# Kernel tuning notes

Hardware: AMD Instinct MI355X
Metric: run time of the kernel (lower is better)

Reference implementation:

```python
import jax, jax.numpy as jnp
import numpy as np

B, S, D_IN, D_EMB, H = 2, 2048, 1024, 1024, 16
HD = D_EMB // H

def setup_inputs() -> dict:
    key = jax.random.key(0)
    k1, k2, k3 = jax.random.split(key, 3)
    # xavier-uniform style scales
    lim_qkv = float(np.sqrt(6.0 / (D_IN + 3 * D_EMB)))
    lim_o = float(np.sqrt(6.0 / (D_EMB + D_EMB)))
    return {
        "x": jax.random.normal(k1, (B, S, D_IN), dtype=jnp.float32),
        "W_qkv": jax.random.uniform(k2, (3 * D_EMB, D_IN), minval=-lim_qkv, maxval=lim_qkv, dtype=jnp.float32),
        "b_qkv": jnp.zeros((3 * D_EMB,), dtype=jnp.float32),
        "W_o": jax.random.uniform(k3, (D_EMB, D_EMB), minval=-lim_o, maxval=lim_o, dtype=jnp.float32),
        "b_o": jnp.zeros((D_EMB,), dtype=jnp.float32),
    }

def reference(x, W_qkv, b_qkv, W_o, b_o):
    b, s, _ = x.shape
    qkv = x @ W_qkv.T + b_qkv                     # [B,S,3E]
    qkv = qkv.reshape(b, s, H, 3 * HD).transpose(0, 2, 1, 3)  # [B,H,S,3*HD]
    q, k, v = jnp.split(qkv, 3, axis=-1)          # each [B,H,S,HD]
    scale = 1.0 / np.sqrt(HD)
    attn = jax.nn.softmax(jnp.einsum('bhqd,bhkd->bhqk', q, k) * scale, axis=-1)
    vals = jnp.einsum('bhqk,bhkd->bhqd', attn, v) # [B,H,S,HD]
    vals = vals.transpose(0, 2, 1, 3).reshape(b, s, D_EMB)
    return vals @ W_o.T + b_o
```

## Files before the change

### kernel.cpp

```cpp
#include <hip/hip_runtime.h>
#include <hip/hip_bf16.h>

typedef unsigned short u16;
typedef unsigned int u32;
typedef __bf16 bf16x8 __attribute__((ext_vector_type(8)));
typedef float f32x4 __attribute__((ext_vector_type(4)));
typedef u32 u32x4 __attribute__((ext_vector_type(4)));

#define MFMA16(a, b, c) __builtin_amdgcn_mfma_f32_16x16x32_bf16((a), (b), (c), 0, 0, 0)

static __device__ __forceinline__ u16 f2bf(float f) {
  __hip_bfloat16 h = __float2bfloat16(f);
  return __builtin_bit_cast(u16, h);
}

static __device__ __forceinline__ u32 pack2(float a, float b) {
  return (u32)f2bf(a) | ((u32)f2bf(b) << 16);
}

static __device__ __forceinline__ bf16x8 ldbf8(const void* p) {
  return *reinterpret_cast<const bf16x8*>(p);
}

static __device__ __forceinline__ void gload_lds16(const void* g, void* l) {
  __builtin_amdgcn_global_load_lds(
      (const __attribute__((address_space(1))) u32*)g,
      (__attribute__((address_space(3))) u32*)l, 16, 0, 0);
}

__global__ void cvt_all(const float* __restrict__ x, const float* __restrict__ wq,
                        const float* __restrict__ wo, u16* __restrict__ xb,
                        u16* __restrict__ wqb, u16* __restrict__ wob) {
  int i = blockIdx.x * 256 + threadIdx.x;
  const float* s;
  u16* d;
  int j;
  if (i < 524288) {
    s = x; d = xb; j = i;
  } else if (i < 917504) {
    s = wq; d = wqb; j = i - 524288;
  } else {
    s = wo; d = wob; j = i - 917504;
  }
  const float4* p = reinterpret_cast<const float4*>(s) + (size_t)j * 2;
  float4 a = p[0], b = p[1];
  uint4 o;
  o.x = (u32)f2bf(a.x) | ((u32)f2bf(a.y) << 16);
  o.y = (u32)f2bf(a.z) | ((u32)f2bf(a.w) << 16);
  o.z = (u32)f2bf(b.x) | ((u32)f2bf(b.y) << 16);
  o.w = (u32)f2bf(b.z) | ((u32)f2bf(b.w) << 16);
  reinterpret_cast<uint4*>(d)[j] = o;
}

template <bool BF16OUT>
__global__ __launch_bounds__(256, 3) void gemm_bt(const u16* __restrict__ A,
                                                  const u16* __restrict__ Bm,
                                                  const float* __restrict__ bias,
                                                  void* __restrict__ Cp,
                                                  int M, int N, int K) {
  __shared__ __align__(16) char As[128 * 64 * 2];
  __shared__ __align__(16) char Bs[128 * 64 * 2];
  const int tid = threadIdx.x;
  const int lane = tid & 63;
  const int wid = tid >> 6;
  const int fr = lane & 15, fg = lane >> 4;
  const int gx = gridDim.x, nwg = gx * gridDim.y;
  const int id = blockIdx.y * gx + blockIdx.x;
  const int nid = (id & 7) * (nwg >> 3) + (id >> 3);
  const int bm = nid / gx, bn = nid % gx;
  const int wm = (wid >> 1) * 64, wn = (wid & 1) * 64;

  f32x4 acc[4][4];
#pragma unroll
  for (int i = 0; i < 4; ++i)
#pragma unroll
    for (int j = 0; j < 4; ++j) acc[i][j] = (f32x4){0.f, 0.f, 0.f, 0.f};

  const int nk = K >> 6;
  for (int kt = 0; kt < nk; ++kt) {
#pragma unroll
    for (int it = 0; it < 4; ++it) {
      int q = it * 256 + tid;
      int row = q >> 3;
      int c = (q & 7) ^ (row & 7);
      gload_lds16(A + (size_t)(bm * 128 + row) * K + kt * 64 + c * 8, As + q * 16);
      gload_lds16(Bm + (size_t)(bn * 128 + row) * K + kt * 64 + c * 8, Bs + q * 16);
    }
    __syncthreads();
#pragma unroll
    for (int mk = 0; mk < 2; ++mk) {
      bf16x8 af[4], bfr[4];
#pragma unroll
      for (int i = 0; i < 4; ++i) {
        int row = wm + i * 16 + fr;
        af[i] = ldbf8(As + ((row * 128 + mk * 64 + fg * 16) ^ ((row & 7) << 4)));
      }
#pragma unroll
      for (int j = 0; j < 4; ++j) {
        int row = wn + j * 16 + fr;
        bfr[j] = ldbf8(Bs + ((row * 128 + mk * 64 + fg * 16) ^ ((row & 7) << 4)));
      }
#pragma unroll
      for (int i = 0; i < 4; ++i)
#pragma unroll
        for (int j = 0; j < 4; ++j) acc[i][j] = MFMA16(af[i], bfr[j], acc[i][j]);
    }
    __syncthreads();
  }

#pragma unroll
  for (int j = 0; j < 4; ++j) {
    int col = bn * 128 + wn + j * 16 + fr;
    float bv = bias[col];
#pragma unroll
    for (int i = 0; i < 4; ++i) {
#pragma unroll
      for (int r = 0; r < 4; ++r) {
        int row = bm * 128 + wm + i * 16 + fg * 4 + r;
        float v = acc[i][j][r] + bv;
        if (BF16OUT)
          ((u16*)Cp)[(size_t)row * N + col] = f2bf(v);
        else
          ((float*)Cp)[(size_t)row * N + col] = v;
      }
    }
  }
}

__global__ __launch_bounds__(256, 2) void gemm_bt64(const u16* __restrict__ A,
                                                    const u16* __restrict__ Bm,
                                                    const float* __restrict__ bias,
                                                    float* __restrict__ Cp,
                                                    int M, int N, int K) {
  __shared__ __align__(16) char As[64 * 64 * 2];
  __shared__ __align__(16) char Bs[128 * 64 * 2];
  const int tid = threadIdx.x;
  const int lane = tid & 63;
  const int wid = tid >> 6;
  const int fr = lane & 15, fg = lane >> 4;
  const int gx = gridDim.x, nwg = gx * gridDim.y;
  const int id = blockIdx.y * gx + blockIdx.x;
  const int nid = (id & 7) * (nwg >> 3) + (id >> 3);
  const int bm = nid / gx, bn = nid % gx;
  const int wm = (wid >> 1) * 32, wn = (wid & 1) * 64;

  f32x4 acc[2][4];
#pragma unroll
  for (int i = 0; i < 2; ++i)
#pragma unroll
    for (int j = 0; j < 4; ++j) acc[i][j] = (f32x4){0.f, 0.f, 0.f, 0.f};

  const int nk = K >> 6;
  for (int kt = 0; kt < nk; ++kt) {
#pragma unroll
    for (int it = 0; it < 2; ++it) {
      int q = it * 256 + tid;
      int row = q >> 3;
      int c = (q & 7) ^ (row & 7);
      gload_lds16(A + (size_t)(bm * 64 + row) * K + kt * 64 + c * 8, As + q * 16);
    }
#pragma unroll
    for (int it = 0; it < 4; ++it) {
      int q = it * 256 + tid;
      int row = q >> 3;
      int c = (q & 7) ^ (row & 7);
      gload_lds16(Bm + (size_t)(bn * 128 + row) * K + kt * 64 + c * 8, Bs + q * 16);
    }
    __syncthreads();
#pragma unroll
    for (int mk = 0; mk < 2; ++mk) {
      bf16x8 af[2], bfr[4];
#pragma unroll
      for (int i = 0; i < 2; ++i) {
        int row = wm + i * 16 + fr;
        af[i] = ldbf8(As + ((row * 128 + mk * 64 + fg * 16) ^ ((row & 7) << 4)));
      }
#pragma unroll
      for (int j = 0; j < 4; ++j) {
        int row = wn + j * 16 + fr;
        bfr[j] = ldbf8(Bs + ((row * 128 + mk * 64 + fg * 16) ^ ((row & 7) << 4)));
      }
#pragma unroll
      for (int i = 0; i < 2; ++i)
#pragma unroll
        for (int j = 0; j < 4; ++j) acc[i][j] = MFMA16(af[i], bfr[j], acc[i][j]);
    }
    __syncthreads();
  }

#pragma unroll
  for (int j = 0; j < 4; ++j) {
    int col = bn * 128 + wn + j * 16 + fr;
    float bv = bias[col];
#pragma unroll
    for (int i = 0; i < 2; ++i) {
#pragma unroll
      for (int r = 0; r < 4; ++r) {
        int row = bm * 64 + wm + i * 16 + fg * 4 + r;
        Cp[(size_t)row * N + col] = acc[i][j][r] + bv;
      }
    }
  }
}

__global__ __launch_bounds__(256, 2) void attn_fwd(const u16* __restrict__ qkv,
                                                   u16* __restrict__ aout) {
  const int id = blockIdx.y * gridDim.x + blockIdx.x;
  const int xcd = id & 7, slot = id >> 3;
  const int bh = xcd * 4 + (slot >> 4);
  const int qt = slot & 15;
  const int b = bh >> 4, h = bh & 15;
  const int tid = threadIdx.x, lane = tid & 63, wid = tid >> 6;
  const int fr = lane & 15, fg = (lane >> 4) & 3;

  __shared__ __align__(16) char Ks[2][2][64 * 128];
  __shared__ __align__(16) char VTs[2][2][64 * 128];

  const int q0 = qt * 128 + wid * 32;
  const size_t bS = (size_t)b * 2048;
  const u16* kbase = qkv + bS * 3072 + h * 192 + 64;
  const u16* vbase = qkv + bS * 3072 + h * 192 + 128;

  const int krow0 = tid >> 3, krow1 = 32 + (tid >> 3);
  const int kcol = (tid & 7) * 8;
  int kw0 = (krow0 * 128 + (tid & 7) * 16) ^ ((krow0 & 7) << 4);
  int kw1 = (krow1 * 128 + (tid & 7) * 16) ^ ((krow1 & 7) << 4);
  asm volatile("" : "+v"(kw0), "+v"(kw1));
  const int vs2 = (tid >> 3) * 2;
  const int vdc = (tid & 7) * 8;
  const int vl0 = 32 * (vs2 >> 5) + 8 * ((vs2 >> 2) & 3) + 4 * ((vs2 >> 4) & 1) +
                  (vs2 & 3);
  int wof[8];
#pragma unroll
  for (int j = 0; j < 8; ++j) {
    int d = vdc + j;
    wof[j] = ((d * 128 + vl0 * 2) ^ ((((d & 7) ^ ((d >> 3) & 7))) << 4));
    asm volatile("" : "+v"(wof[j]));
  }
  int kro[2];
#pragma unroll
  for (int mk = 0; mk < 2; ++mk) {
    kro[mk] = ((fr * 128 + mk * 64 + fg * 16) ^ ((fr & 7) << 4));
    asm volatile("" : "+v"(kro[mk]));
  }
  int vadr[4][2];
#pragma unroll
  for (int tp = 0; tp < 4; ++tp)
#pragma unroll
    for (int mk = 0; mk < 2; ++mk) {
      int d = tp * 16 + fr;
      int swz = (((d & 7) ^ ((d >> 3) & 7)) << 4);
      vadr[tp][mk] = ((d * 128 + mk * 64 + fg * 16) ^ swz);
      asm volatile("" : "+v"(vadr[tp][mk]));
    }

  bf16x8 qf[2][2];
#pragma unroll
  for (int qs = 0; qs < 2; ++qs)
#pragma unroll
    for (int mk = 0; mk < 2; ++mk) {
      bf16x8 v =
          ldbf8(qkv + (bS + q0 + qs * 16 + fr) * 3072 + h * 192 + mk * 32 + fg * 8);
#pragma unroll
      for (int e = 0; e < 8; ++e) v[e] = (__bf16)((float)v[e] * 0.1803368801f);
      qf[qs][mk] = v;
    }

  const u32 one2 = 0x3F803F80u;
  const u32x4 onev = {one2, one2, one2, one2};
  const bf16x8 onesf = __builtin_bit_cast(bf16x8, onev);
  float zs = 0.f;
  asm volatile("" : "+v"(zs));
  const f32x4 zacc = {zs, zs, zs, zs};

  f32x4 oacc0[4], oacc1[4];
#pragma unroll
  for (int t = 0; t < 4; ++t) {
    oacc0[t] = (f32x4){0.f, 0.f, 0.f, 0.f};
    oacc1[t] = (f32x4){0.f, 0.f, 0.f, 0.f};
  }
  f32x4 lacc0 = (f32x4){0.f, 0.f, 0.f, 0.f};
  f32x4 lacc1 = (f32x4){0.f, 0.f, 0.f, 0.f};

#define LOADT(S0, K0, K1, K2, K3, V0, V1, V2, V3)                                         \
  K0 = *reinterpret_cast<const uint4*>(kbase + (size_t)((S0) + krow0) * 3072 + kcol);      \
  K1 = *reinterpret_cast<const uint4*>(kbase + (size_t)((S0) + krow1) * 3072 + kcol);      \
  K2 = *reinterpret_cast<const uint4*>(kbase + (size_t)((S0) + 64 + krow0) * 3072 + kcol); \
  K3 = *reinterpret_cast<const uint4*>(kbase + (size_t)((S0) + 64 + krow1) * 3072 + kcol); \
  V0 = *reinterpret_cast<const uint4*>(vbase + (size_t)((S0) + vs2) * 3072 + vdc);         \
  V1 = *reinterpret_cast<const uint4*>(vbase + (size_t)((S0) + vs2 + 1) * 3072 + vdc);     \
  V2 = *reinterpret_cast<const uint4*>(vbase + (size_t)((S0) + 64 + vs2) * 3072 + vdc);    \
  V3 = *reinterpret_cast<const uint4*>(vbase + (size_t)((S0) + 64 + vs2 + 1) * 3072 + vdc);

#define STAGEV1(VTP, V0, V1)                           \
  {                                                    \
    const u16* e0 = reinterpret_cast<const u16*>(&V0); \
    const u16* e1 = reinterpret_cast<const u16*>(&V1); \
    _Pragma("unroll") for (int j = 0; j < 8; ++j) {    \
      u32 w = (u32)e0[j] | ((u32)e1[j] << 16);         \
      *reinterpret_cast<u32*>((VTP) + wof[j]) = w;     \
    }                                                  \
  }

#define STAGE(BUF, K0, K1, K2, K3, V0, V1, V2, V3)        \
  {                                                       \
    *reinterpret_cast<uint4*>(Ks[BUF][0] + kw0) = K0;     \
    *reinterpret_cast<uint4*>(Ks[BUF][0] + kw1) = K1;     \
    *reinterpret_cast<uint4*>(Ks[BUF][1] + kw0) = K2;     \
    *reinterpret_cast<uint4*>(Ks[BUF][1] + kw1) = K3;     \
    STAGEV1(VTs[BUF][0], V0, V1);                         \
    STAGEV1(VTs[BUF][1], V2, V3);                         \
  }

#define BAR()                                          \
  {                                                    \
    __builtin_amdgcn_sched_barrier(0);                 \
    asm volatile("s_waitcnt lgkmcnt(0)" ::: "memory"); \
    __builtin_amdgcn_s_barrier();                      \
    __builtin_amdgcn_sched_barrier(0);                 \
  }

#define COMPUTE1(KSP, VTP)                                                     \
  {                                                                            \
    f32x4 sc0[4], sc1[4];                                                      \
    __builtin_amdgcn_s_setprio(1);                                             \
    _Pragma("unroll") for (int t = 0; t < 4; ++t) {                            \
      bf16x8 kf0 = ldbf8((KSP) + kro[0] + t * 2048);                           \
      bf16x8 kf1 = ldbf8((KSP) + kro[1] + t * 2048);                           \
      sc0[t] = MFMA16(kf0, qf[0][0], zacc);                                    \
      sc0[t] = MFMA16(kf1, qf[0][1], sc0[t]);                                  \
      sc1[t] = MFMA16(kf0, qf[1][0], zacc);                                    \
      sc1[t] = MFMA16(kf1, qf[1][1], sc1[t]);                                  \
    }                                                                          \
    __builtin_amdgcn_s_setprio(0);                                             \
    u32 Wp0[2][4], Wp1[2][4];                                                  \
    _Pragma("unroll") for (int t = 0; t < 4; ++t) {                            \
      Wp0[0][t] = pack2(__builtin_amdgcn_exp2f(sc0[t][0]),                     \
                        __builtin_amdgcn_exp2f(sc0[t][1]));                    \
      Wp0[1][t] = pack2(__builtin_amdgcn_exp2f(sc0[t][2]),                     \
                        __builtin_amdgcn_exp2f(sc0[t][3]));                    \
      Wp1[0][t] = pack2(__builtin_amdgcn_exp2f(sc1[t][0]),                     \
                        __builtin_amdgcn_exp2f(sc1[t][1]));                    \
      Wp1[1][t] = pack2(__builtin_amdgcn_exp2f(sc1[t][2]),                     \
                        __builtin_amdgcn_exp2f(sc1[t][3]));                    \
    }                                                                          \
    _Pragma("unroll") for (int mk = 0; mk < 2; ++mk) {                         \
      u32x4 pk0, pk1;                                                          \
      pk0.x = Wp0[0][2 * mk];                                                  \
      pk0.y = Wp0[1][2 * mk];                                                  \
      pk0.z = Wp0[0][2 * mk + 1];                                              \
      pk0.w = Wp0[1][2 * mk + 1];                                              \
      pk1.x = Wp1[0][2 * mk];                                                  \
      pk1.y = Wp1[1][2 * mk];                                                  \
      pk1.z = Wp1[0][2 * mk + 1];                                              \
      pk1.w = Wp1[1][2 * mk + 1];                                              \
      bf16x8 pa0 = __builtin_bit_cast(bf16x8, pk0);                            \
      bf16x8 pa1 = __builtin_bit_cast(bf16x8, pk1);                            \
      __builtin_amdgcn_s_setprio(1);                                           \
      lacc0 = MFMA16(pa0, onesf, lacc0);                                       \
      lacc1 = MFMA16(pa1, onesf, lacc1);                                       \
      _Pragma("unroll") for (int tp = 0; tp < 4; ++tp) {                       \
        bf16x8 vf = ldbf8((VTP) + vadr[tp][mk]);                               \
        oacc0[tp] = MFMA16(pa0, vf, oacc0[tp]);                                \
        oacc1[tp] = MFMA16(pa1, vf, oacc1[tp]);                                \
      }                                                                        \
      __builtin_amdgcn_s_setprio(0);                                           \
    }                                                                          \
  }

#define COMPUTE(BUF)                   \
  {                                    \
    COMPUTE1(Ks[BUF][0], VTs[BUF][0]); \
    COMPUTE1(Ks[BUF][1], VTs[BUF][1]); \
  }

  uint4 ka0, ka1, ka2, ka3, va0, va1, va2, va3;
  uint4 kb0, kb1, kb2, kb3, vb0, vb1, vb2, vb3;
  LOADT(0, ka0, ka1, ka2, ka3, va0, va1, va2, va3);
  STAGE(0, ka0, ka1, ka2, ka3, va0, va1, va2, va3);
  LOADT(128, kb0, kb1, kb2, kb3, vb0, vb1, vb2, vb3);
  BAR();
  for (int kv = 0; kv < 16; kv += 2) {
    {
      int s0n = (kv + 2 < 16) ? (kv + 2) * 128 : 0;
      LOADT(s0n, ka0, ka1, ka2, ka3, va0, va1, va2, va3);
    }
    STAGE(1, kb0, kb1, kb2, kb3, vb0, vb1, vb2, vb3);
    COMPUTE(0);
    BAR();
    {
      int s0n = (kv + 3 < 16) ? (kv + 3) * 128 : 128;
      LOADT(s0n, kb0, kb1, kb2, kb3, vb0, vb1, vb2, vb3);
    }
    STAGE(0, ka0, ka1, ka2, ka3, va0, va1, va2, va3);
    COMPUTE(1);
    BAR();
  }
#undef LOADT
#undef STAGEV1
#undef STAGE
#undef BAR
#undef COMPUTE1
#undef COMPUTE

  {
    float invb0[4], invb1[4];
#pragma unroll
    for (int r = 0; r < 4; ++r) {
      invb0[r] = 1.f / lacc0[r];
      invb1[r] = 1.f / lacc1[r];
    }
#pragma unroll
    for (int tp = 0; tp < 4; ++tp) {
#pragma unroll
      for (int r = 0; r < 4; ++r) {
        int row0 = q0 + fg * 4 + r;
        aout[(bS + row0) * 1024 + h * 64 + tp * 16 + fr] =
            f2bf(oacc0[tp][r] * invb0[r]);
        int row1 = q0 + 16 + fg * 4 + r;
        aout[(bS + row1) * 1024 + h * 64 + tp * 16 + fr] =
            f2bf(oacc1[tp][r] * invb1[r]);
      }
    }
  }
}

extern "C" void kernel_launch(void* const* d_in, const int* in_sizes, int n_in,
                              void* d_out, int out_size, void* d_ws, size_t ws_size,
                              hipStream_t stream) {
  const float* x = (const float*)d_in[0];
  const float* Wqkv = (const float*)d_in[1];
  const float* bqkv = (const float*)d_in[2];
  const float* Wo = (const float*)d_in[3];
  const float* bo = (const float*)d_in[4];
  float* out = (float*)d_out;
  char* ws = (char*)d_ws;

  u16* xb = (u16*)(ws);
  u16* wqb = (u16*)(ws + 8388608);
  u16* wob = (u16*)(ws + 14680064);
  u16* qkvb = (u16*)(ws + 16777216);
  u16* attb = (u16*)(ws + 41943040);

  cvt_all<<<4096, 256, 0, stream>>>(x, Wqkv, Wo, xb, wqb, wob);

  gemm_bt<true><<<dim3(24, 32), 256, 0, stream>>>(xb, wqb, bqkv, qkvb, 4096, 3072, 1024);
  attn_fwd<<<dim3(16, 32), 256, 0, stream>>>(qkvb, attb);
  gemm_bt64<<<dim3(8, 64), 256, 0, stream>>>(attb, wob, bo, out, 4096, 1024, 1024);
}
```

Baseline: 103.4 us.

## Load K tiles directly into LDS with async global-to-LDS copies

K tiles are now fetched with direct global-to-LDS loads (gload_lds16), using an XOR swizzle applied on the global column, instead of being loaded into registers and then stored to LDS. V still goes through registers for the transpose. The barrier waits with vmcnt(4) so that only the outstanding V register loads stay in flight. This is meant to cut VGPR pressure and LDS store instructions, but it relies on the vmcnt count being correct for the K copies to be complete before compute reads them.

```diff
diff --git a/kernel.cpp b/kernel.cpp
--- a/kernel.cpp
+++ b/kernel.cpp
@@ -221,11 +221,6 @@
   const u16* kbase = qkv + bS * 3072 + h * 192 + 64;
   const u16* vbase = qkv + bS * 3072 + h * 192 + 128;
 
-  const int krow0 = tid >> 3, krow1 = 32 + (tid >> 3);
-  const int kcol = (tid & 7) * 8;
-  int kw0 = (krow0 * 128 + (tid & 7) * 16) ^ ((krow0 & 7) << 4);
-  int kw1 = (krow1 * 128 + (tid & 7) * 16) ^ ((krow1 & 7) << 4);
-  asm volatile("" : "+v"(kw0), "+v"(kw1));
   const int vs2 = (tid >> 3) * 2;
   const int vdc = (tid & 7) * 8;
   const int vl0 = 32 * (vs2 >> 5) + 8 * ((vs2 >> 2) & 3) + 4 * ((vs2 >> 4) & 1) +
@@ -282,14 +277,21 @@
   f32x4 lacc0 = (f32x4){0.f, 0.f, 0.f, 0.f};
   f32x4 lacc1 = (f32x4){0.f, 0.f, 0.f, 0.f};
 
-#define LOADT(S0, K0, K1, K2, K3, V0, V1, V2, V3)                                         \
-  K0 = *reinterpret_cast<const uint4*>(kbase + (size_t)((S0) + krow0) * 3072 + kcol);      \
-  K1 = *reinterpret_cast<const uint4*>(kbase + (size_t)((S0) + krow1) * 3072 + kcol);      \
-  K2 = *reinterpret_cast<const uint4*>(kbase + (size_t)((S0) + 64 + krow0) * 3072 + kcol); \
-  K3 = *reinterpret_cast<const uint4*>(kbase + (size_t)((S0) + 64 + krow1) * 3072 + kcol); \
-  V0 = *reinterpret_cast<const uint4*>(vbase + (size_t)((S0) + vs2) * 3072 + vdc);         \
-  V1 = *reinterpret_cast<const uint4*>(vbase + (size_t)((S0) + vs2 + 1) * 3072 + vdc);     \
-  V2 = *reinterpret_cast<const uint4*>(vbase + (size_t)((S0) + 64 + vs2) * 3072 + vdc);    \
+#define KISSUE(S0, BUF)                                                        \
+  _Pragma("unroll") for (int it = 0; it < 2; ++it) {                           \
+    int q = it * 256 + tid;                                                    \
+    int row = q >> 3;                                                          \
+    int c = (q & 7) ^ (row & 7);                                               \
+    gload_lds16(kbase + (size_t)((S0) + row) * 3072 + c * 8,                   \
+                Ks[BUF][0] + q * 16);                                          \
+    gload_lds16(kbase + (size_t)((S0) + 64 + row) * 3072 + c * 8,              \
+                Ks[BUF][1] + q * 16);                                          \
+  }
+
+#define LOADV(S0, V0, V1, V2, V3)                                                  \
+  V0 = *reinterpret_cast<const uint4*>(vbase + (size_t)((S0) + vs2) * 3072 + vdc); \
+  V1 = *reinterpret_cast<const uint4*>(vbase + (size_t)((S0) + vs2 + 1) * 3072 + vdc); \
+  V2 = *reinterpret_cast<const uint4*>(vbase + (size_t)((S0) + 64 + vs2) * 3072 + vdc); \
   V3 = *reinterpret_cast<const uint4*>(vbase + (size_t)((S0) + 64 + vs2 + 1) * 3072 + vdc);
 
 #define STAGEV1(VTP, V0, V1)                           \
@@ -302,22 +304,18 @@
     }                                                  \
   }
 
-#define STAGE(BUF, K0, K1, K2, K3, V0, V1, V2, V3)        \
-  {                                                       \
-    *reinterpret_cast<uint4*>(Ks[BUF][0] + kw0) = K0;     \
-    *reinterpret_cast<uint4*>(Ks[BUF][0] + kw1) = K1;     \
-    *reinterpret_cast<uint4*>(Ks[BUF][1] + kw0) = K2;     \
-    *reinterpret_cast<uint4*>(Ks[BUF][1] + kw1) = K3;     \
-    STAGEV1(VTs[BUF][0], V0, V1);                         \
-    STAGEV1(VTs[BUF][1], V2, V3);                         \
-  }
-
-#define BAR()                                          \
-  {                                                    \
-    __builtin_amdgcn_sched_barrier(0);                 \
-    asm volatile("s_waitcnt lgkmcnt(0)" ::: "memory"); \
-    __builtin_amdgcn_s_barrier();                      \
-    __builtin_amdgcn_sched_barrier(0);                 \
+#define STAGEV(BUF, V0, V1, V2, V3)   \
+  {                                   \
+    STAGEV1(VTs[BUF][0], V0, V1);     \
+    STAGEV1(VTs[BUF][1], V2, V3);     \
+  }
+
+#define BARC()                                                   \
+  {                                                              \
+    __builtin_amdgcn_sched_barrier(0);                           \
+    asm volatile("s_waitcnt vmcnt(4) lgkmcnt(0)" ::: "memory");  \
+    __builtin_amdgcn_s_barrier();                                \
+    __builtin_amdgcn_sched_barrier(0);                           \
   }
 
 #define COMPUTE1(KSP, VTP)                                                     \
@@ -374,32 +372,45 @@
     COMPUTE1(Ks[BUF][1], VTs[BUF][1]); \
   }
 
-  uint4 ka0, ka1, ka2, ka3, va0, va1, va2, va3;
-  uint4 kb0, kb1, kb2, kb3, vb0, vb1, vb2, vb3;
-  LOADT(0, ka0, ka1, ka2, ka3, va0, va1, va2, va3);
-  STAGE(0, ka0, ka1, ka2, ka3, va0, va1, va2, va3);
-  LOADT(128, kb0, kb1, kb2, kb3, vb0, vb1, vb2, vb3);
-  BAR();
+  uint4 va0, va1, va2, va3;
+  uint4 vb0, vb1, vb2, vb3;
+  KISSUE(0, 0);
+  __builtin_amdgcn_sched_barrier(0);
+  LOADV(0, va0, va1, va2, va3);
+  STAGEV(0, va0, va1, va2, va3);
+  LOADV(128, vb0, vb1, vb2, vb3);
+  BARC();
   for (int kv = 0; kv < 16; kv += 2) {
     {
-      int s0n = (kv + 2 < 16) ? (kv + 2) * 128 : 0;
-      LOADT(s0n, ka0, ka1, ka2, ka3, va0, va1, va2, va3);
-    }
-    STAGE(1, kb0, kb1, kb2, kb3, vb0, vb1, vb2, vb3);
+      int sk = (kv + 1 < 16) ? (kv + 1) * 128 : 0;
+      KISSUE(sk, 1);
+    }
+    __builtin_amdgcn_sched_barrier(0);
+    {
+      int sv = (kv + 2 < 16) ? (kv + 2) * 128 : 0;
+      LOADV(sv, va0, va1, va2, va3);
+    }
+    STAGEV(1, vb0, vb1, vb2, vb3);
     COMPUTE(0);
-    BAR();
+    BARC();
     {
-      int s0n = (kv + 3 < 16) ? (kv + 3) * 128 : 128;
-      LOADT(s0n, kb0, kb1, kb2, kb3, vb0, vb1, vb2, vb3);
-    }
-    STAGE(0, ka0, ka1, ka2, ka3, va0, va1, va2, va3);
+      int sk = (kv + 2 < 16) ? (kv + 2) * 128 : 0;
+      KISSUE(sk, 0);
+    }
+    __builtin_amdgcn_sched_barrier(0);
+    {
+      int sv = (kv + 3 < 16) ? (kv + 3) * 128 : 128;
+      LOADV(sv, vb0, vb1, vb2, vb3);
+    }
+    STAGEV(0, va0, va1, va2, va3);
     COMPUTE(1);
-    BAR();
-  }
-#undef LOADT
+    BARC();
+  }
+#undef KISSUE
+#undef LOADV
 #undef STAGEV1
-#undef STAGE
-#undef BAR
+#undef STAGEV
+#undef BARC
 #undef COMPUTE1
 #undef COMPUTE
 
```

Measured after the change: 102.7 us, median of 2. About the same (-0.6%).
